# Performance work log

Hardware: AMD Instinct MI355X
Metric: run time of the kernel (lower is better)

The kernel has to match this reference:

```python
import jax, jax.numpy as jnp
import numpy as np

NMS_KS = 15
TOP_K = 2048
GAUSS_KS = 7
GAUSS_SIGMA = 1.0
LOSS_LAMBDA = 1.0


def setup_inputs() -> dict:
    key = jax.random.key(0)
    k1, k2, k3 = jax.random.split(key, 3)
    B, H, W = 16, 1024, 1024
    score1 = jax.random.uniform(k1, (B, 1, H, W), dtype=jnp.float32)
    w_score2 = jax.random.uniform(k2, (B, 1, H, W), dtype=jnp.float32)
    w_vis_mask2 = jax.random.randint(k3, (B, 1, H, W), 0, 2) > 0
    return {"score1": score1, "w_score2": w_score2, "w_vis_mask2": w_vis_mask2}


def _nms(score, ks):
    # keep only local maxima within a ks x ks window (stride 1, 'same' padding)
    pooled = jax.lax.reduce_window(score, -jnp.inf, jax.lax.max,
                                   (1, 1, ks, ks), (1, 1, 1, 1), 'SAME')
    return jnp.where(score == pooled, score, jnp.zeros_like(score))


def _prepare_gt_score(score, nms_ks, k, mask):
    # NMS -> mask -> per-image top-k -> binary GT keypoint map
    s = _nms(score, nms_ks) * mask.astype(score.dtype)
    b = s.shape[0]
    flat = s.reshape(b, -1)                      # B x (H*W)
    _, idx = jax.lax.top_k(flat, k)              # B x k
    gt = jnp.zeros_like(flat).at[jnp.arange(b)[:, None], idx].set(1.0)
    return gt.reshape(s.shape)


def _gaussian_filter(x, ks, sigma):
    coords = jnp.arange(ks, dtype=jnp.float32) - (ks - 1) / 2.0
    g = jnp.exp(-(coords ** 2) / (2.0 * sigma ** 2))
    g = g / g.sum()
    k2d = jnp.outer(g, g)[None, None]
    pad = ks // 2
    return jax.lax.conv_general_dilated(
        x, k2d, (1, 1), [(pad, pad), (pad, pad)],
        dimension_numbers=('NCHW', 'OIHW', 'NCHW'))


def reference(score1, w_score2, w_vis_mask2):
    b = score1.shape[0]
    gt_score1 = jax.lax.stop_gradient(
        _prepare_gt_score(w_score2, NMS_KS, TOP_K, w_vis_mask2))
    gt_score1 = _gaussian_filter(gt_score1, GAUSS_KS, GAUSS_SIGMA)
    m = w_vis_mask2.astype(jnp.float32)
    loss = ((score1 - gt_score1) ** 2) * m       # masked elementwise MSE
    loss = loss.reshape(b, -1).sum(-1) / jnp.clip(m.reshape(b, -1).sum(-1), 1e-8)
    return LOSS_LAMBDA * loss.mean()
```

## Files before the change

kernel.cpp:

```cpp
#include <hip/hip_runtime.h>
#include <math.h>

#define BATCH 16
#define H 1024
#define W 1024
#define HR 46
#define CGW 20
#define CGP 21
#define NTILES 8192
#define NBANDS (NTILES * 4)
#define CAP 4096
#define TOPK 2048
#define BCW 12

struct WS {
  double term1[BATCH];
  double corr[BATCH];
  unsigned int masksum[BATCH];
  int cand_count[BATCH];
  int   band_cnt[NBANDS];
  float pt1[NBANDS];
  int   pmc[NBANDS];
  float band_val[NBANDS * BCW];
  int   band_idx[NBANDS * BCW];
  float ccand_val[BATCH * CAP];
  int   ccand_idx[BATCH * CAP];
};

__constant__ float GW[7] = {
  0.004433048175f, 0.054005582623f, 0.242036229376f, 0.399050279652f,
  0.242036229376f, 0.054005582623f, 0.004433048175f
};

__device__ __forceinline__ float4 max4(float4 a, float4 b) {
  float4 r;
  r.x = fmaxf(a.x, b.x); r.y = fmaxf(a.y, b.y);
  r.z = fmaxf(a.z, b.z); r.w = fmaxf(a.w, b.w);
  return r;
}

__global__ __launch_bounds__(256, 6) void k_nms(const float* __restrict__ score1,
                                                const float* __restrict__ score2,
                                                const int* __restrict__ mask,
                                                WS* __restrict__ ws) {
  __shared__ float4 halo[HR][CGP];
  __shared__ float4 rmax[32][CGP];
  const int tid = threadIdx.x;

  const int t = (blockIdx.x & 7) * (NTILES / 8) + (blockIdx.x >> 3);
  const int b  = t >> 9;
  const int tt = t & 511;
  const int ty0 = (tt >> 4) << 5;
  const int tx0 = (tt & 15) << 6;
  const size_t ibase = (size_t)b * ((size_t)H * W);

  float4 st[4];
  int hr_[4], hc_[4];
  const bool interior = (ty0 >= 7) && (ty0 + 38 < H) && (tx0 >= 8) && (tx0 + 71 < W);
  if (interior) {
    #pragma unroll
    for (int k = 0; k < 4; k++) {
      int i = tid + (k << 8);
      if (i < HR * CGW) {
        int r = i / CGW, c = i - r * CGW;
        hr_[k] = r; hc_[k] = c;
        st[k] = *((const float4*)(score2 + ibase + (size_t)(ty0 - 7 + r) * W + (tx0 - 8)) + c);
      }
    }
  } else {
    #pragma unroll
    for (int k = 0; k < 4; k++) {
      int i = tid + (k << 8);
      if (i < HR * CGW) {
        int r = i / CGW, c = i - r * CGW;
        hr_[k] = r; hc_[k] = c;
        int gy = ty0 - 7 + r, gx = tx0 - 8 + (c << 2);
        float vv[4] = {-INFINITY, -INFINITY, -INFINITY, -INFINITY};
        if (gy >= 0 && gy < H) {
          const float* rp = score2 + ibase + (size_t)gy * W;
          #pragma unroll
          for (int u = 0; u < 4; u++) {
            int gxu = gx + u;
            if (gxu >= 0 && gxu < W) vv[u] = rp[gxu];
          }
        }
        st[k] = make_float4(vv[0], vv[1], vv[2], vv[3]);
      }
    }
  }
  const int w  = tid >> 6;
  const int l  = tid & 63;
  const int rt = (w << 3) + (l >> 3);
  const int c8 = l & 7;
  const size_t pb = ibase + (size_t)(ty0 + rt) * W + tx0 + (c8 << 3);
  const float4 s1a = *(const float4*)(score1 + pb);
  const float4 s1b = *(const float4*)(score1 + pb + 4);
  const int4  mka = *(const int4*)(mask + pb);
  const int4  mkb = *(const int4*)(mask + pb + 4);

  #pragma unroll
  for (int k = 0; k < 4; k++) {
    int i = tid + (k << 8);
    if (i < HR * CGW) halo[hr_[k]][hc_[k]] = st[k];
  }

  float t1 = 0.f; int mcnt = 0; unsigned int mbits = 0;
  {
    const float sc[8] = {s1a.x, s1a.y, s1a.z, s1a.w, s1b.x, s1b.y, s1b.z, s1b.w};
    const int   mm[8] = {mka.x, mka.y, mka.z, mka.w, mkb.x, mkb.y, mkb.z, mkb.w};
    #pragma unroll
    for (int j = 0; j < 8; j++) {
      if (mm[j]) { t1 = fmaf(sc[j], sc[j], t1); mcnt++; mbits |= (1u << j); }
    }
  }
  __syncthreads();

  if (l < 40) {
    const int r2 = l / 20;
    const int cg = l - r2 * 20;
    const int R0 = (w << 3) + (r2 << 2);
    float4 core = halo[R0 + 3][cg];
    #pragma unroll
    for (int k = 4; k <= 14; k++) core = max4(core, halo[R0 + k][cg]);
    const float4 h0 = halo[R0][cg], h1 = halo[R0 + 1][cg], h2 = halo[R0 + 2][cg];
    const float4 h15 = halo[R0 + 15][cg], h16 = halo[R0 + 16][cg], h17 = halo[R0 + 17][cg];
    const float4 p2 = h2, p1 = max4(h1, p2), p0 = max4(h0, p1);
    const float4 sf15 = h15, sf16 = max4(sf15, h16), sf17 = max4(sf16, h17);
    rmax[R0 + 0][cg] = max4(core, p0);
    rmax[R0 + 1][cg] = max4(max4(core, p1), sf15);
    rmax[R0 + 2][cg] = max4(max4(core, p2), sf16);
    rmax[R0 + 3][cg] = max4(core, sf17);
  }
  __builtin_amdgcn_wave_barrier();
  asm volatile("s_waitcnt lgkmcnt(0)" ::: "memory");
  __builtin_amdgcn_sched_barrier(0);

  float r[24];
  #pragma unroll
  for (int g = 0; g < 6; g++) {
    float4 v = rmax[rt][(c8 << 1) + g];
    r[4 * g + 0] = v.x; r[4 * g + 1] = v.y; r[4 * g + 2] = v.z; r[4 * g + 3] = v.w;
  }
  float core = r[8];
  #pragma unroll
  for (int k = 9; k <= 15; k++) core = fmaxf(core, r[k]);
  const float q7 = r[7];
  const float q6 = fmaxf(r[6], q7);
  const float q5 = fmaxf(r[5], q6);
  const float q4 = fmaxf(r[4], q5);
  const float q3 = fmaxf(r[3], q4);
  const float q2 = fmaxf(r[2], q3);
  const float q1 = fmaxf(r[1], q2);
  float sa[7];
  sa[0] = r[16];
  #pragma unroll
  for (int k = 1; k < 7; k++) sa[k] = fmaxf(sa[k - 1], r[16 + k]);
  float pooled[8];
  pooled[0] = fmaxf(core, q1);
  pooled[1] = fmaxf(fmaxf(core, q2), sa[0]);
  pooled[2] = fmaxf(fmaxf(core, q3), sa[1]);
  pooled[3] = fmaxf(fmaxf(core, q4), sa[2]);
  pooled[4] = fmaxf(fmaxf(core, q5), sa[3]);
  pooled[5] = fmaxf(fmaxf(core, q6), sa[4]);
  pooled[6] = fmaxf(fmaxf(core, q7), sa[5]);
  pooled[7] = fmaxf(core, sa[6]);

  const float4 cva = halo[rt + 7][(c8 << 1) + 2];
  const float4 cvb = halo[rt + 7][(c8 << 1) + 3];
  const float cc[8] = {cva.x, cva.y, cva.z, cva.w, cvb.x, cvb.y, cvb.z, cvb.w};
  int   cj = -1; float cv = 0.f;
  #pragma unroll
  for (int j = 0; j < 8; j++) {
    if (((mbits >> j) & 1u) && cj < 0) {
      const float s = cc[j];
      if (s == pooled[j] && s > 0.f) { cj = j; cv = s; }
    }
  }
  const int band = (t << 2) + w;
  const unsigned long long bal = __ballot(cj >= 0);
  if (cj >= 0) {
    const int pos = (int)__popcll(bal & ((1ull << l) - 1ull));
    if (pos < BCW) {
      ws->band_val[band * BCW + pos] = cv;
      ws->band_idx[band * BCW + pos] = (ty0 + rt) * W + tx0 + (c8 << 3) + cj;
    }
  }
  #pragma unroll
  for (int off = 32; off > 0; off >>= 1) {
    t1 += __shfl_down(t1, off);
    mcnt += __shfl_down(mcnt, off);
  }
  if (l == 0) {
    int nc = (int)__popcll(bal); if (nc > BCW) nc = BCW;
    ws->band_cnt[band] = nc;
    ws->pt1[band] = t1;
    ws->pmc[band] = mcnt;
  }
}

__global__ __launch_bounds__(256) void k_compact(WS* __restrict__ ws) {
  const int b = blockIdx.x;
  const int tid = threadIdx.x;
  const int lane = tid & 63, w = tid >> 6;
  __shared__ double sF[4];
  __shared__ int    sI[4];
  __shared__ int    wt[4];

  double tsum = 0.0; int msum = 0;
  for (int j = tid; j < 2048; j += 256) {
    tsum += (double)ws->pt1[b * 2048 + j];
    msum += ws->pmc[b * 2048 + j];
  }
  #pragma unroll
  for (int off = 32; off > 0; off >>= 1) {
    tsum += __shfl_down(tsum, off);
    msum += __shfl_down(msum, off);
  }
  if (lane == 0) { sF[w] = tsum; sI[w] = msum; }

  const int base = b * 2048 + tid * 8;
  int c[8]; int csum = 0;
  #pragma unroll
  for (int u = 0; u < 8; u++) {
    int x = ws->band_cnt[base + u];
    if (x > BCW) x = BCW;
    c[u] = x; csum += x;
  }
  int v = csum;
  #pragma unroll
  for (int off = 1; off < 64; off <<= 1) {
    int u = __shfl_up(v, off);
    if (lane >= off) v += u;
  }
  if (lane == 63) wt[w] = v;
  __syncthreads();
  if (tid == 0) {
    ws->term1[b] = (sF[0] + sF[1]) + (sF[2] + sF[3]);
    ws->masksum[b] = (unsigned int)(sI[0] + sI[1] + sI[2] + sI[3]);
    ws->corr[b] = 0.0;
  }
  int wo = 0;
  #pragma unroll
  for (int k = 0; k < 4; k++) if (k < w) wo += wt[k];
  const int excl = v - csum + wo;
  float* dv = ws->ccand_val + b * CAP;
  int*   di = ws->ccand_idx + b * CAP;
  if (tid == 255) {
    int tot = excl + csum;
    if (tot > CAP) tot = CAP;
    ws->cand_count[b] = tot;
    #pragma unroll
    for (int u = 0; u < 3; u++)
      if (tot + u < CAP) dv[tot + u] = 0.f;
  }
  int off = excl;
  #pragma unroll
  for (int u = 0; u < 8; u++) {
    const float* sv = ws->band_val + (size_t)(base + u) * BCW;
    const int*   si = ws->band_idx + (size_t)(base + u) * BCW;
    for (int j = 0; j < c[u]; j++) {
      if (off < CAP) { dv[off] = sv[j]; di[off] = si[j]; }
      off++;
    }
  }
}

__global__ __launch_bounds__(256, 4) void k_rankstamp(const float* __restrict__ score1,
                                                      const int* __restrict__ mask,
                                                      WS* __restrict__ ws) {
  const int blk = (blockIdx.x & 7) * 128 + (blockIdx.x >> 3);
  const int b = blk >> 6;
  const int slice = blk & 63;
  int n = ws->cand_count[b]; if (n > CAP) n = CAP;
  const int i0 = slice << 6;
  if (i0 >= n) return;
  __shared__ __align__(16) float sval[CAP];
  __shared__ __align__(16) int   sidx[CAP];
  __shared__ int   s_prank[4][64];
  __shared__ int   s_keys[64];
  __shared__ int   s_nk;
  __shared__ float cred[4];
  const int tid = threadIdx.x;
  const int nf4 = (n + 3) >> 2;

  const float4* gv = (const float4*)(ws->ccand_val + b * CAP);
  const int4*   gi = (const int4*)(ws->ccand_idx + b * CAP);
  for (int j = tid; j < nf4; j += 256) {
    ((float4*)sval)[j] = gv[j];
    ((int4*)sidx)[j]   = gi[j];
  }
  __syncthreads();

  const int w = tid >> 6, l = tid & 63;
  const float vi = sval[i0 + l];
  const int   xi = sidx[i0 + l];
  const int q = (nf4 + 3) >> 2;
  int lo = w * q; if (lo > nf4) lo = nf4;
  int hi = lo + q; if (hi > nf4) hi = nf4;
  int rank = 0;
  int j = lo;
  for (; j + 4 <= hi; j += 4) {
    #pragma unroll
    for (int u = 0; u < 4; u++) {
      const float4 v = ((const float4*)sval)[j + u];
      const int4  iv = ((const int4*)sidx)[j + u];
      rank += (v.x > vi) + (v.y > vi) + (v.z > vi) + (v.w > vi);
      rank += (v.x == vi && iv.x < xi);
      rank += (v.y == vi && iv.y < xi);
      rank += (v.z == vi && iv.z < xi);
      rank += (v.w == vi && iv.w < xi);
    }
  }
  for (; j < hi; j++) {
    const float4 v = ((const float4*)sval)[j];
    const int4  iv = ((const int4*)sidx)[j];
    rank += (v.x > vi) + (v.y > vi) + (v.z > vi) + (v.w > vi);
    rank += (v.x == vi && iv.x < xi);
    rank += (v.y == vi && iv.y < xi);
    rank += (v.z == vi && iv.z < xi);
    rank += (v.w == vi && iv.w < xi);
  }
  s_prank[w][l] = rank;
  __syncthreads();

  if (tid < 64) {
    const int rtot = s_prank[0][tid] + s_prank[1][tid] + s_prank[2][tid] + s_prank[3][tid];
    const bool sel = (i0 + tid < n) && (rtot < TOPK);
    const unsigned long long bal = __ballot(sel);
    if (sel) {
      const int pos = __popcll(bal & ((1ull << tid) - 1ull));
      s_keys[pos] = sidx[i0 + tid];
    }
    if (tid == 0) s_nk = (int)__popcll(bal);
  }
  __syncthreads();
  const int nk = s_nk;

  float contrib = 0.f;
  const int sub = tid & 7;
  const size_t ib2 = (size_t)b * ((size_t)H * W);
  #pragma unroll
  for (int rnd = 0; rnd < 2; rnd++) {
    const int k = (tid >> 3) + (rnd << 5);
    if (k < nk && sub < 7) {
      const int ck = s_keys[k];
      const int cy = ck >> 10, cx = ck & 1023;
      const int py = cy + sub - 3;
      const float wy = GW[sub] * ((py >= 0 && py < H) ? 1.f : 0.f);
      const int pyc = min(max(py, 0), H - 1);
      const float* s1r = score1 + ib2 + (size_t)pyc * W;
      const int*   mr  = mask   + ib2 + (size_t)pyc * W;
      #pragma unroll
      for (int dx = -3; dx <= 3; dx++) {
        const int px = cx + dx;
        const float wv = wy * GW[dx + 3] * ((px >= 0 && px < W) ? 1.f : 0.f);
        const int pxc = min(max(px, 0), W - 1);
        const float mf = (mr[pxc] != 0) ? 1.f : 0.f;
        contrib += mf * wv * (wv - 2.f * s1r[pxc]);
      }
    }
  }
  #pragma unroll
  for (int off = 32; off > 0; off >>= 1) contrib += __shfl_down(contrib, off);
  if ((tid & 63) == 0) cred[tid >> 6] = contrib;
  __syncthreads();
  if (tid == 0)
    atomicAdd(&ws->corr[b], (double)((cred[0] + cred[1]) + (cred[2] + cred[3])));
}

__global__ void k_final(WS* __restrict__ ws, float* __restrict__ out) {
  const int t = threadIdx.x;
  double v = 0.0;
  if (t < BATCH) {
    double denom = (double)ws->masksum[t];
    if (denom < 1e-8) denom = 1e-8;
    v = (ws->term1[t] + ws->corr[t]) / denom;
  }
  #pragma unroll
  for (int off = 32; off > 0; off >>= 1) v += __shfl_down(v, off);
  if (t == 0) out[0] = (float)(v / BATCH);
}

extern "C" void kernel_launch(void* const* d_in, const int* in_sizes, int n_in,
                              void* d_out, int out_size, void* d_ws, size_t ws_size,
                              hipStream_t stream) {
  const float* score1 = (const float*)d_in[0];
  const float* score2 = (const float*)d_in[1];
  const int*   mask   = (const int*)d_in[2];
  float* out = (float*)d_out;
  WS* ws = (WS*)d_ws;

  k_nms<<<NTILES, 256, 0, stream>>>(score1, score2, mask, ws);
  k_compact<<<BATCH, 256, 0, stream>>>(ws);
  k_rankstamp<<<BATCH * 64, 256, 0, stream>>>(score1, mask, ws);
  k_final<<<1, 64, 0, stream>>>(ws, out);
}
```

Before: 85.82 us.

## Process two vertically stacked NMS tiles per block with software-pipelined halo loads

Each k_nms block now handles two 32-row tiles instead of one, halving the grid to 4096 blocks. The second tile's global halo, score1 and mask loads are issued before the first tile's vertical and horizontal max passes, so memory latency overlaps with compute. The vertical pass is redistributed across 160 threads with block-level syncs instead of per-wave barriers. This costs extra registers (launch bound occupancy hint lowered from 6 to 5) and adds more __syncthreads per block.

Measured after the change: 88.41 us. +3.0%, slower.

```diff
diff --git a/kernel.cpp b/kernel.cpp
--- a/kernel.cpp
+++ b/kernel.cpp
@@ -9,6 +9,7 @@
 #define CGP 21
 #define NTILES 8192
 #define NBANDS (NTILES * 4)
+#define NBLK 4096
 #define CAP 4096
 #define TOPK 2048
 #define BCW 12
@@ -39,23 +40,9 @@
   return r;
 }
 
-__global__ __launch_bounds__(256, 6) void k_nms(const float* __restrict__ score1,
-                                                const float* __restrict__ score2,
-                                                const int* __restrict__ mask,
-                                                WS* __restrict__ ws) {
-  __shared__ float4 halo[HR][CGP];
-  __shared__ float4 rmax[32][CGP];
-  const int tid = threadIdx.x;
-
-  const int t = (blockIdx.x & 7) * (NTILES / 8) + (blockIdx.x >> 3);
-  const int b  = t >> 9;
-  const int tt = t & 511;
-  const int ty0 = (tt >> 4) << 5;
-  const int tx0 = (tt & 15) << 6;
-  const size_t ibase = (size_t)b * ((size_t)H * W);
-
-  float4 st[4];
-  int hr_[4], hc_[4];
+__device__ __forceinline__ void halo_issue(const float* __restrict__ src,
+                                           int ty0, int tx0, int tid,
+                                           float4 st[4], int hr_[4], int hc_[4]) {
   const bool interior = (ty0 >= 7) && (ty0 + 38 < H) && (tx0 >= 8) && (tx0 + 71 < W);
   if (interior) {
     #pragma unroll
@@ -64,7 +51,7 @@
       if (i < HR * CGW) {
         int r = i / CGW, c = i - r * CGW;
         hr_[k] = r; hc_[k] = c;
-        st[k] = *((const float4*)(score2 + ibase + (size_t)(ty0 - 7 + r) * W + (tx0 - 8)) + c);
+        st[k] = *((const float4*)(src + (size_t)(ty0 - 7 + r) * W + (tx0 - 8)) + c);
       }
     }
   } else {
@@ -77,7 +64,7 @@
         int gy = ty0 - 7 + r, gx = tx0 - 8 + (c << 2);
         float vv[4] = {-INFINITY, -INFINITY, -INFINITY, -INFINITY};
         if (gy >= 0 && gy < H) {
-          const float* rp = score2 + ibase + (size_t)gy * W;
+          const float* rp = src + (size_t)gy * W;
           #pragma unroll
           for (int u = 0; u < 4; u++) {
             int gxu = gx + u;
@@ -88,37 +75,13 @@
       }
     }
   }
-  const int w  = tid >> 6;
-  const int l  = tid & 63;
-  const int rt = (w << 3) + (l >> 3);
-  const int c8 = l & 7;
-  const size_t pb = ibase + (size_t)(ty0 + rt) * W + tx0 + (c8 << 3);
-  const float4 s1a = *(const float4*)(score1 + pb);
-  const float4 s1b = *(const float4*)(score1 + pb + 4);
-  const int4  mka = *(const int4*)(mask + pb);
-  const int4  mkb = *(const int4*)(mask + pb + 4);
-
-  #pragma unroll
-  for (int k = 0; k < 4; k++) {
-    int i = tid + (k << 8);
-    if (i < HR * CGW) halo[hr_[k]][hc_[k]] = st[k];
-  }
-
-  float t1 = 0.f; int mcnt = 0; unsigned int mbits = 0;
-  {
-    const float sc[8] = {s1a.x, s1a.y, s1a.z, s1a.w, s1b.x, s1b.y, s1b.z, s1b.w};
-    const int   mm[8] = {mka.x, mka.y, mka.z, mka.w, mkb.x, mkb.y, mkb.z, mkb.w};
-    #pragma unroll
-    for (int j = 0; j < 8; j++) {
-      if (mm[j]) { t1 = fmaf(sc[j], sc[j], t1); mcnt++; mbits |= (1u << j); }
-    }
-  }
-  __syncthreads();
-
-  if (l < 40) {
-    const int r2 = l / 20;
-    const int cg = l - r2 * 20;
-    const int R0 = (w << 3) + (r2 << 2);
+}
+
+__device__ __forceinline__ void vpass(const float4 (*halo)[CGP], float4 (*rmax)[CGP], int tid) {
+  if (tid < 160) {
+    const int rr = tid / 20;
+    const int cg = tid - rr * 20;
+    const int R0 = rr << 2;
     float4 core = halo[R0 + 3][cg];
     #pragma unroll
     for (int k = 4; k <= 14; k++) core = max4(core, halo[R0 + k][cg]);
@@ -131,10 +94,14 @@
     rmax[R0 + 2][cg] = max4(max4(core, p2), sf16);
     rmax[R0 + 3][cg] = max4(core, sf17);
   }
-  __builtin_amdgcn_wave_barrier();
-  asm volatile("s_waitcnt lgkmcnt(0)" ::: "memory");
-  __builtin_amdgcn_sched_barrier(0);
-
+}
+
+__device__ __forceinline__ void hpass_emit(const float4 (*rmax)[CGP],
+                                           float4 cva, float4 cvb,
+                                           unsigned int mbits, float t1, int mcnt,
+                                           int tile, int ty0, int tx0,
+                                           int rt, int c8, int w, int l,
+                                           WS* __restrict__ ws) {
   float r[24];
   #pragma unroll
   for (int g = 0; g < 6; g++) {
@@ -165,10 +132,8 @@
   pooled[6] = fmaxf(fmaxf(core, q7), sa[5]);
   pooled[7] = fmaxf(core, sa[6]);
 
-  const float4 cva = halo[rt + 7][(c8 << 1) + 2];
-  const float4 cvb = halo[rt + 7][(c8 << 1) + 3];
   const float cc[8] = {cva.x, cva.y, cva.z, cva.w, cvb.x, cvb.y, cvb.z, cvb.w};
-  int   cj = -1; float cv = 0.f;
+  int cj = -1; float cv = 0.f;
   #pragma unroll
   for (int j = 0; j < 8; j++) {
     if (((mbits >> j) & 1u) && cj < 0) {
@@ -176,7 +141,7 @@
       if (s == pooled[j] && s > 0.f) { cj = j; cv = s; }
     }
   }
-  const int band = (t << 2) + w;
+  const int band = (tile << 2) + w;
   const unsigned long long bal = __ballot(cj >= 0);
   if (cj >= 0) {
     const int pos = (int)__popcll(bal & ((1ull << l) - 1ull));
@@ -196,6 +161,95 @@
     ws->pt1[band] = t1;
     ws->pmc[band] = mcnt;
   }
+}
+
+__global__ __launch_bounds__(256, 5) void k_nms(const float* __restrict__ score1,
+                                                const float* __restrict__ score2,
+                                                const int* __restrict__ mask,
+                                                WS* __restrict__ ws) {
+  __shared__ float4 halo[HR][CGP];
+  __shared__ float4 rmax[32][CGP];
+  const int tid = threadIdx.x;
+  const int w = tid >> 6, l = tid & 63;
+
+  const int g  = (blockIdx.x & 7) * (NBLK / 8) + (blockIdx.x >> 3);
+  const int b  = g >> 8;
+  const int gg = g & 255;
+  const int rp = gg >> 4;
+  const int cI = gg & 15;
+  const int tx0 = cI << 6;
+  const int ty0A = rp << 6;
+  const int ty0B = ty0A + 32;
+  const size_t ibase = (size_t)b * ((size_t)H * W);
+  const float* s2 = score2 + ibase;
+  const int tileA = (b << 9) + ((rp << 1) << 4) + cI;
+  const int tileB = tileA + 16;
+
+  const int rt = (w << 3) + (l >> 3);
+  const int c8 = l & 7;
+
+  float4 stA[4]; int hrA[4], hcA[4];
+  halo_issue(s2, ty0A, tx0, tid, stA, hrA, hcA);
+  const size_t pbA = ibase + (size_t)(ty0A + rt) * W + tx0 + (c8 << 3);
+  const float4 s1aA = *(const float4*)(score1 + pbA);
+  const float4 s1bA = *(const float4*)(score1 + pbA + 4);
+  const int4  mkaA = *(const int4*)(mask + pbA);
+  const int4  mkbA = *(const int4*)(mask + pbA + 4);
+
+  float t1A = 0.f; int mcntA = 0; unsigned int mbitsA = 0;
+  {
+    const float sc[8] = {s1aA.x, s1aA.y, s1aA.z, s1aA.w, s1bA.x, s1bA.y, s1bA.z, s1bA.w};
+    const int   mm[8] = {mkaA.x, mkaA.y, mkaA.z, mkaA.w, mkbA.x, mkbA.y, mkbA.z, mkbA.w};
+    #pragma unroll
+    for (int j = 0; j < 8; j++) {
+      if (mm[j]) { t1A = fmaf(sc[j], sc[j], t1A); mcntA++; mbitsA |= (1u << j); }
+    }
+  }
+  #pragma unroll
+  for (int k = 0; k < 4; k++) {
+    int i = tid + (k << 8);
+    if (i < HR * CGW) halo[hrA[k]][hcA[k]] = stA[k];
+  }
+  __syncthreads();
+
+  float4 stB[4]; int hrB[4], hcB[4];
+  halo_issue(s2, ty0B, tx0, tid, stB, hrB, hcB);
+  const size_t pbB = pbA + (size_t)32 * W;
+  const float4 s1aB = *(const float4*)(score1 + pbB);
+  const float4 s1bB = *(const float4*)(score1 + pbB + 4);
+  const int4  mkaB = *(const int4*)(mask + pbB);
+  const int4  mkbB = *(const int4*)(mask + pbB + 4);
+  __builtin_amdgcn_sched_barrier(0);
+
+  vpass(halo, rmax, tid);
+  const float4 cvaA = halo[rt + 7][(c8 << 1) + 2];
+  const float4 cvbA = halo[rt + 7][(c8 << 1) + 3];
+  __syncthreads();
+
+  hpass_emit(rmax, cvaA, cvbA, mbitsA, t1A, mcntA, tileA, ty0A, tx0, rt, c8, w, l, ws);
+
+  #pragma unroll
+  for (int k = 0; k < 4; k++) {
+    int i = tid + (k << 8);
+    if (i < HR * CGW) halo[hrB[k]][hcB[k]] = stB[k];
+  }
+  float t1B = 0.f; int mcntB = 0; unsigned int mbitsB = 0;
+  {
+    const float sc[8] = {s1aB.x, s1aB.y, s1aB.z, s1aB.w, s1bB.x, s1bB.y, s1bB.z, s1bB.w};
+    const int   mm[8] = {mkaB.x, mkaB.y, mkaB.z, mkaB.w, mkbB.x, mkbB.y, mkbB.z, mkbB.w};
+    #pragma unroll
+    for (int j = 0; j < 8; j++) {
+      if (mm[j]) { t1B = fmaf(sc[j], sc[j], t1B); mcntB++; mbitsB |= (1u << j); }
+    }
+  }
+  __syncthreads();
+
+  vpass(halo, rmax, tid);
+  const float4 cvaB = halo[rt + 7][(c8 << 1) + 2];
+  const float4 cvbB = halo[rt + 7][(c8 << 1) + 3];
+  __syncthreads();
+
+  hpass_emit(rmax, cvaB, cvbB, mbitsB, t1B, mcntB, tileB, ty0B, tx0, rt, c8, w, l, ws);
 }
 
 __global__ __launch_bounds__(256) void k_compact(WS* __restrict__ ws) {
@@ -390,7 +444,7 @@
   float* out = (float*)d_out;
   WS* ws = (WS*)d_ws;
 
-  k_nms<<<NTILES, 256, 0, stream>>>(score1, score2, mask, ws);
+  k_nms<<<NBLK, 256, 0, stream>>>(score1, score2, mask, ws);
   k_compact<<<BATCH, 256, 0, stream>>>(ws);
   k_rankstamp<<<BATCH * 64, 256, 0, stream>>>(score1, mask, ws);
   k_final<<<1, 64, 0, stream>>>(ws, out);
```

## Fold candidate compaction into rank kernel and move per-image reductions to final kernel

Applied to the files above, without the earlier changes.

Removes the separate compaction kernel. Each rank-stamp block now recomputes the prefix scan over band counts and gathers candidates straight into shared memory. The term1 and mask-count reductions move into a widened final kernel, and the double atomics are replaced by per-slice partial sums. The NMS halo load is also unified into one clamped float4 path with no interior/border branch. This saves a launch and a global round trip, at the cost of 64 blocks per image each redoing the scan and gather from the band buffers.

New measurement: 88.34 us. +2.9%, slower.

```diff
diff --git a/kernel.cpp b/kernel.cpp
--- a/kernel.cpp
+++ b/kernel.cpp
@@ -14,17 +14,12 @@
 #define BCW 12
 
 struct WS {
-  double term1[BATCH];
-  double corr[BATCH];
-  unsigned int masksum[BATCH];
-  int cand_count[BATCH];
-  int   band_cnt[NBANDS];
   float pt1[NBANDS];
   int   pmc[NBANDS];
+  int   band_cnt[NBANDS];
+  float corr_part[BATCH * 64];
   float band_val[NBANDS * BCW];
   int   band_idx[NBANDS * BCW];
-  float ccand_val[BATCH * CAP];
-  int   ccand_idx[BATCH * CAP];
 };
 
 __constant__ float GW[7] = {
@@ -46,6 +41,7 @@
   __shared__ float4 halo[HR][CGP];
   __shared__ float4 rmax[32][CGP];
   const int tid = threadIdx.x;
+  const int w = tid >> 6, l = tid & 63;
 
   const int t = (blockIdx.x & 7) * (NTILES / 8) + (blockIdx.x >> 3);
   const int b  = t >> 9;
@@ -53,43 +49,24 @@
   const int ty0 = (tt >> 4) << 5;
   const int tx0 = (tt & 15) << 6;
   const size_t ibase = (size_t)b * ((size_t)H * W);
-
-  float4 st[4];
-  int hr_[4], hc_[4];
-  const bool interior = (ty0 >= 7) && (ty0 + 38 < H) && (tx0 >= 8) && (tx0 + 71 < W);
-  if (interior) {
-    #pragma unroll
-    for (int k = 0; k < 4; k++) {
-      int i = tid + (k << 8);
-      if (i < HR * CGW) {
-        int r = i / CGW, c = i - r * CGW;
-        hr_[k] = r; hc_[k] = c;
-        st[k] = *((const float4*)(score2 + ibase + (size_t)(ty0 - 7 + r) * W + (tx0 - 8)) + c);
-      }
-    }
-  } else {
-    #pragma unroll
-    for (int k = 0; k < 4; k++) {
-      int i = tid + (k << 8);
-      if (i < HR * CGW) {
-        int r = i / CGW, c = i - r * CGW;
-        hr_[k] = r; hc_[k] = c;
-        int gy = ty0 - 7 + r, gx = tx0 - 8 + (c << 2);
-        float vv[4] = {-INFINITY, -INFINITY, -INFINITY, -INFINITY};
-        if (gy >= 0 && gy < H) {
-          const float* rp = score2 + ibase + (size_t)gy * W;
-          #pragma unroll
-          for (int u = 0; u < 4; u++) {
-            int gxu = gx + u;
-            if (gxu >= 0 && gxu < W) vv[u] = rp[gxu];
-          }
-        }
-        st[k] = make_float4(vv[0], vv[1], vv[2], vv[3]);
-      }
-    }
-  }
-  const int w  = tid >> 6;
-  const int l  = tid & 63;
+  const float* s2 = score2 + ibase;
+
+  float4 st[4]; int hr_[4], hc_[4];
+  #pragma unroll
+  for (int k = 0; k < 4; k++) {
+    int i = tid + (k << 8);
+    if (i < HR * CGW) {
+      int r = i / CGW, c = i - r * CGW;
+      hr_[k] = r; hc_[k] = c;
+      int gy = ty0 - 7 + r, gx = tx0 - 8 + (c << 2);
+      const bool ok = (gy >= 0) & (gy < H) & (gx >= 0) & (gx < W);
+      int gyc = min(max(gy, 0), H - 1);
+      int gxc = ok ? gx : 0;
+      float4 v = *(const float4*)(s2 + (size_t)gyc * W + gxc);
+      if (!ok) v = make_float4(-INFINITY, -INFINITY, -INFINITY, -INFINITY);
+      st[k] = v;
+    }
+  }
   const int rt = (w << 3) + (l >> 3);
   const int c8 = l & 7;
   const size_t pb = ibase + (size_t)(ty0 + rt) * W + tx0 + (c8 << 3);
@@ -168,7 +145,7 @@
   const float4 cva = halo[rt + 7][(c8 << 1) + 2];
   const float4 cvb = halo[rt + 7][(c8 << 1) + 3];
   const float cc[8] = {cva.x, cva.y, cva.z, cva.w, cvb.x, cvb.y, cvb.z, cvb.w};
-  int   cj = -1; float cv = 0.f;
+  int cj = -1; float cv = 0.f;
   #pragma unroll
   for (int j = 0; j < 8; j++) {
     if (((mbits >> j) & 1u) && cj < 0) {
@@ -198,100 +175,71 @@
   }
 }
 
-__global__ __launch_bounds__(256) void k_compact(WS* __restrict__ ws) {
-  const int b = blockIdx.x;
-  const int tid = threadIdx.x;
-  const int lane = tid & 63, w = tid >> 6;
-  __shared__ double sF[4];
-  __shared__ int    sI[4];
-  __shared__ int    wt[4];
-
-  double tsum = 0.0; int msum = 0;
-  for (int j = tid; j < 2048; j += 256) {
-    tsum += (double)ws->pt1[b * 2048 + j];
-    msum += ws->pmc[b * 2048 + j];
-  }
-  #pragma unroll
-  for (int off = 32; off > 0; off >>= 1) {
-    tsum += __shfl_down(tsum, off);
-    msum += __shfl_down(msum, off);
-  }
-  if (lane == 0) { sF[w] = tsum; sI[w] = msum; }
-
-  const int base = b * 2048 + tid * 8;
-  int c[8]; int csum = 0;
-  #pragma unroll
-  for (int u = 0; u < 8; u++) {
-    int x = ws->band_cnt[base + u];
-    if (x > BCW) x = BCW;
-    c[u] = x; csum += x;
-  }
-  int v = csum;
-  #pragma unroll
-  for (int off = 1; off < 64; off <<= 1) {
-    int u = __shfl_up(v, off);
-    if (lane >= off) v += u;
-  }
-  if (lane == 63) wt[w] = v;
-  __syncthreads();
-  if (tid == 0) {
-    ws->term1[b] = (sF[0] + sF[1]) + (sF[2] + sF[3]);
-    ws->masksum[b] = (unsigned int)(sI[0] + sI[1] + sI[2] + sI[3]);
-    ws->corr[b] = 0.0;
-  }
-  int wo = 0;
-  #pragma unroll
-  for (int k = 0; k < 4; k++) if (k < w) wo += wt[k];
-  const int excl = v - csum + wo;
-  float* dv = ws->ccand_val + b * CAP;
-  int*   di = ws->ccand_idx + b * CAP;
-  if (tid == 255) {
-    int tot = excl + csum;
-    if (tot > CAP) tot = CAP;
-    ws->cand_count[b] = tot;
-    #pragma unroll
-    for (int u = 0; u < 3; u++)
-      if (tot + u < CAP) dv[tot + u] = 0.f;
-  }
-  int off = excl;
-  #pragma unroll
-  for (int u = 0; u < 8; u++) {
-    const float* sv = ws->band_val + (size_t)(base + u) * BCW;
-    const int*   si = ws->band_idx + (size_t)(base + u) * BCW;
-    for (int j = 0; j < c[u]; j++) {
-      if (off < CAP) { dv[off] = sv[j]; di[off] = si[j]; }
-      off++;
-    }
-  }
-}
-
 __global__ __launch_bounds__(256, 4) void k_rankstamp(const float* __restrict__ score1,
                                                       const int* __restrict__ mask,
                                                       WS* __restrict__ ws) {
   const int blk = (blockIdx.x & 7) * 128 + (blockIdx.x >> 3);
   const int b = blk >> 6;
   const int slice = blk & 63;
-  int n = ws->cand_count[b]; if (n > CAP) n = CAP;
-  const int i0 = slice << 6;
-  if (i0 >= n) return;
   __shared__ __align__(16) float sval[CAP];
   __shared__ __align__(16) int   sidx[CAP];
+  __shared__ int   wt[4];
+  __shared__ int   s_tot;
   __shared__ int   s_prank[4][64];
   __shared__ int   s_keys[64];
   __shared__ int   s_nk;
   __shared__ float cred[4];
   const int tid = threadIdx.x;
+  const int w = tid >> 6, l = tid & 63;
+
+  const int base = b * 2048 + tid * 8;
+  int c[8]; int csum = 0;
+  #pragma unroll
+  for (int u = 0; u < 8; u++) {
+    int x = ws->band_cnt[base + u];
+    if (x > BCW) x = BCW;
+    c[u] = x; csum += x;
+  }
+  int v = csum;
+  #pragma unroll
+  for (int off = 1; off < 64; off <<= 1) {
+    int u2 = __shfl_up(v, off);
+    if (l >= off) v += u2;
+  }
+  if (l == 63) wt[w] = v;
+  __syncthreads();
+  int wo = 0;
+  #pragma unroll
+  for (int k = 0; k < 4; k++) if (k < w) wo += wt[k];
+  const int excl = v - csum + wo;
+  if (tid == 255) {
+    int tot = excl + csum;
+    if (tot > CAP) tot = CAP;
+    s_tot = tot;
+    #pragma unroll
+    for (int u = 0; u < 3; u++)
+      if (tot + u < CAP) sval[tot + u] = 0.f;
+  }
+  int off = excl;
+  #pragma unroll
+  for (int u = 0; u < 8; u++) {
+    const float* sv = ws->band_val + (size_t)(base + u) * BCW;
+    const int*   si = ws->band_idx + (size_t)(base + u) * BCW;
+    for (int j = 0; j < c[u]; j++) {
+      if (off < CAP) { sval[off] = sv[j]; sidx[off] = si[j]; }
+      off++;
+    }
+  }
+  __syncthreads();
+
+  const int n = s_tot;
+  const int i0 = slice << 6;
+  if (i0 >= n) {
+    if (tid == 0) ws->corr_part[b * 64 + slice] = 0.f;
+    return;
+  }
   const int nf4 = (n + 3) >> 2;
 
-  const float4* gv = (const float4*)(ws->ccand_val + b * CAP);
-  const int4*   gi = (const int4*)(ws->ccand_idx + b * CAP);
-  for (int j = tid; j < nf4; j += 256) {
-    ((float4*)sval)[j] = gv[j];
-    ((int4*)sidx)[j]   = gi[j];
-  }
-  __syncthreads();
-
-  const int w = tid >> 6, l = tid & 63;
   const float vi = sval[i0 + l];
   const int   xi = sidx[i0 + l];
   const int q = (nf4 + 3) >> 2;
@@ -302,23 +250,23 @@
   for (; j + 4 <= hi; j += 4) {
     #pragma unroll
     for (int u = 0; u < 4; u++) {
-      const float4 v = ((const float4*)sval)[j + u];
+      const float4 vv = ((const float4*)sval)[j + u];
       const int4  iv = ((const int4*)sidx)[j + u];
-      rank += (v.x > vi) + (v.y > vi) + (v.z > vi) + (v.w > vi);
-      rank += (v.x == vi && iv.x < xi);
-      rank += (v.y == vi && iv.y < xi);
-      rank += (v.z == vi && iv.z < xi);
-      rank += (v.w == vi && iv.w < xi);
+      rank += (vv.x > vi) + (vv.y > vi) + (vv.z > vi) + (vv.w > vi);
+      rank += (vv.x == vi && iv.x < xi);
+      rank += (vv.y == vi && iv.y < xi);
+      rank += (vv.z == vi && iv.z < xi);
+      rank += (vv.w == vi && iv.w < xi);
     }
   }
   for (; j < hi; j++) {
-    const float4 v = ((const float4*)sval)[j];
+    const float4 vv = ((const float4*)sval)[j];
     const int4  iv = ((const int4*)sidx)[j];
-    rank += (v.x > vi) + (v.y > vi) + (v.z > vi) + (v.w > vi);
-    rank += (v.x == vi && iv.x < xi);
-    rank += (v.y == vi && iv.y < xi);
-    rank += (v.z == vi && iv.z < xi);
-    rank += (v.w == vi && iv.w < xi);
+    rank += (vv.x > vi) + (vv.y > vi) + (vv.z > vi) + (vv.w > vi);
+    rank += (vv.x == vi && iv.x < xi);
+    rank += (vv.y == vi && iv.y < xi);
+    rank += (vv.z == vi && iv.z < xi);
+    rank += (vv.w == vi && iv.w < xi);
   }
   s_prank[w][l] = rank;
   __syncthreads();
@@ -361,24 +309,47 @@
     }
   }
   #pragma unroll
-  for (int off = 32; off > 0; off >>= 1) contrib += __shfl_down(contrib, off);
-  if ((tid & 63) == 0) cred[tid >> 6] = contrib;
+  for (int off2 = 32; off2 > 0; off2 >>= 1) contrib += __shfl_down(contrib, off2);
+  if (l == 0) cred[w] = contrib;
   __syncthreads();
   if (tid == 0)
-    atomicAdd(&ws->corr[b], (double)((cred[0] + cred[1]) + (cred[2] + cred[3])));
-}
-
-__global__ void k_final(WS* __restrict__ ws, float* __restrict__ out) {
-  const int t = threadIdx.x;
-  double v = 0.0;
-  if (t < BATCH) {
-    double denom = (double)ws->masksum[t];
+    ws->corr_part[b * 64 + slice] = (cred[0] + cred[1]) + (cred[2] + cred[3]);
+}
+
+__global__ __launch_bounds__(1024) void k_final(WS* __restrict__ ws, float* __restrict__ out) {
+  const int tid = threadIdx.x;
+  const int b = tid >> 6, l = tid & 63;
+  __shared__ double sD[BATCH];
+
+  double tsum = 0.0; long long msum = 0;
+  const float4* pv = (const float4*)(ws->pt1 + b * 2048);
+  const int4*   pm = (const int4*)(ws->pmc + b * 2048);
+  #pragma unroll
+  for (int k = 0; k < 8; k++) {
+    const float4 f = pv[l + (k << 6)];
+    const int4   m = pm[l + (k << 6)];
+    tsum += (double)f.x + (double)f.y + (double)f.z + (double)f.w;
+    msum += (long long)(m.x + m.y + m.z + m.w);
+  }
+  double csum = (double)ws->corr_part[b * 64 + l];
+  #pragma unroll
+  for (int off = 32; off > 0; off >>= 1) {
+    tsum += __shfl_down(tsum, off);
+    msum += __shfl_down(msum, off);
+    csum += __shfl_down(csum, off);
+  }
+  if (l == 0) {
+    double denom = (double)msum;
     if (denom < 1e-8) denom = 1e-8;
-    v = (ws->term1[t] + ws->corr[t]) / denom;
-  }
-  #pragma unroll
-  for (int off = 32; off > 0; off >>= 1) v += __shfl_down(v, off);
-  if (t == 0) out[0] = (float)(v / BATCH);
+    sD[b] = (tsum + csum) / denom;
+  }
+  __syncthreads();
+  if (tid == 0) {
+    double acc = 0.0;
+    #pragma unroll
+    for (int k = 0; k < BATCH; k++) acc += sD[k];
+    out[0] = (float)(acc / BATCH);
+  }
 }
 
 extern "C" void kernel_launch(void* const* d_in, const int* in_sizes, int n_in,
@@ -391,7 +362,6 @@
   WS* ws = (WS*)d_ws;
 
   k_nms<<<NTILES, 256, 0, stream>>>(score1, score2, mask, ws);
-  k_compact<<<BATCH, 256, 0, stream>>>(ws);
   k_rankstamp<<<BATCH * 64, 256, 0, stream>>>(score1, mask, ws);
-  k_final<<<1, 64, 0, stream>>>(ws, out);
-}
+  k_final<<<1, 1024, 0, stream>>>(ws, out);
+}
```
